# Optimization experiments

Measured on AMD Instinct MI355X. Metric: run time of the kernel, lower is better.

Reference implementation:

```python
import jax, jax.numpy as jnp
import numpy as np

B, T, C, H = 2, 2048, 2048, 16
DH = C // H  # 128
INNER = 4 * C  # 8192
EPS = 1e-5


def _ln(x, w, b):
    mu = jnp.mean(x, axis=-1, keepdims=True)
    var = jnp.mean((x - mu) ** 2, axis=-1, keepdims=True)
    return (x - mu) * jax.lax.rsqrt(var + EPS) * w + b


def _apply_rotary(x, cos, sin):
    # x: [B,H,T,DH]; cos/sin: [T,DH//2] broadcast over B,H
    x1 = x[..., ::2]
    x2 = x[..., 1::2]
    r = jnp.stack([x1 * cos - x2 * sin, x1 * sin + x2 * cos], axis=-1)
    return r.reshape(r.shape[:-2] + (-1,))


def setup_inputs() -> dict:
    key = jax.random.key(0)
    ks = jax.random.split(key, 8)
    std = 0.02
    x = jax.random.normal(ks[0], (B, T, C), dtype=jnp.float32)
    # RoPE tables
    inv_freq = 1.0 / (10000.0 ** (np.arange(0, DH, 2, dtype=np.float32) / DH))
    ang = np.arange(T, dtype=np.float32)[:, None] * inv_freq[None, :]  # [T, DH//2]
    cos = jnp.asarray(np.cos(ang))
    sin = jnp.asarray(np.sin(ang))
    return {
        "x": x,
        "cos": cos,
        "sin": sin,
        "ln1_w": jnp.ones((C,), jnp.float32),
        "ln1_b": jnp.zeros((C,), jnp.float32),
        "ln2_w": jnp.ones((C,), jnp.float32),
        "ln2_b": jnp.zeros((C,), jnp.float32),
        "W_qkv": jax.random.normal(ks[1], (C, 3 * C), jnp.float32) * std,
        "W_o": jax.random.normal(ks[2], (C, C), jnp.float32) * std,
        "W1": jax.random.normal(ks[3], (C, INNER), jnp.float32) * std,
        "W2": jax.random.normal(ks[4], (C, INNER), jnp.float32) * std,
        "W3": jax.random.normal(ks[5], (INNER, C), jnp.float32) * std,
    }


def reference(x, cos, sin, ln1_w, ln1_b, ln2_w, ln2_b, W_qkv, W_o, W1, W2, W3):
    # --- attention sub-block (pre-LN) ---
    a = _ln(x, ln1_w, ln1_b)
    qkv = a @ W_qkv  # [B,T,3C]
    q, k, v = jnp.split(qkv, 3, axis=-1)
    q = q.reshape(B, T, H, DH).transpose(0, 2, 1, 3)  # [B,H,T,DH]
    k = k.reshape(B, T, H, DH).transpose(0, 2, 1, 3)
    v = v.reshape(B, T, H, DH).transpose(0, 2, 1, 3)
    q = _apply_rotary(q, cos, sin)
    k = _apply_rotary(k, cos, sin)
    scores = jnp.einsum("bhtd,bhsd->bhts", q, k) / jnp.sqrt(jnp.float32(DH))
    mask = jnp.triu(jnp.full((T, T), -jnp.inf, dtype=scores.dtype), k=1)
    scores = scores + mask
    attn = jax.nn.softmax(scores, axis=-1)
    y = jnp.einsum("bhts,bhsd->bhtd", attn, v)
    y = y.transpose(0, 2, 1, 3).reshape(B, T, C) @ W_o
    x = x + y
    # --- SwiGLU MLP sub-block (pre-LN) ---
    h = _ln(x, ln2_w, ln2_b)
    m = (jax.nn.silu(h @ W1) * (h @ W2)) @ W3
    return x + m
```

## Files before the change

### kernel.cpp

```cpp
#include <hip/hip_runtime.h>
#include <hip/hip_bf16.h>
#include <cstdint>

#define DEVINL __device__ __forceinline__

using f32x4  = __attribute__((ext_vector_type(4))) float;
using short8 = __attribute__((ext_vector_type(8))) short;
using short4v = __attribute__((ext_vector_type(4))) short;

DEVINL float bf2f(__hip_bfloat16 h){ return __bfloat162float(h); }
DEVINL __hip_bfloat16 f2bf(float f){ return __float2bfloat16(f); }
DEVINL short bfbits(float f){ __hip_bfloat16 h = __float2bfloat16(f); short s; __builtin_memcpy(&s, &h, 2); return s; }
DEVINL float sb2f(short s){ uint32_t u = ((uint32_t)(uint16_t)s) << 16; float f; __builtin_memcpy(&f, &u, 4); return f; }

DEVINL void gl_lds16(const void* g, void* l){
  __builtin_amdgcn_global_load_lds((const __attribute__((address_space(1))) void*)g,
                                   (__attribute__((address_space(3))) void*)l, 16, 0, 0);
}

__global__ __launch_bounds__(256) void wtrans(const float* __restrict__ src,
                                              __hip_bfloat16* __restrict__ dst,
                                              int R, int C){
  __shared__ float tile[32][33];
  const int tr0 = blockIdx.y*32, tc0 = blockIdx.x*32;
  const int t = threadIdx.x;
  const int lr = t >> 3, lc = (t & 7) * 4;
  float4 v = *(const float4*)(src + (size_t)(tr0+lr)*C + tc0 + lc);
  tile[lr][lc] = v.x; tile[lr][lc+1] = v.y; tile[lr][lc+2] = v.z; tile[lr][lc+3] = v.w;
  __syncthreads();
  short4v o;
  o[0] = bfbits(tile[lc+0][lr]);
  o[1] = bfbits(tile[lc+1][lr]);
  o[2] = bfbits(tile[lc+2][lr]);
  o[3] = bfbits(tile[lc+3][lr]);
  *(short4v*)(dst + (size_t)(tc0+lr)*R + tr0 + lc) = o;
}

__global__ __launch_bounds__(256) void ln_k(const float* __restrict__ x,
                                            const float* __restrict__ w,
                                            const float* __restrict__ bia,
                                            __hip_bfloat16* __restrict__ out){
  const int row = blockIdx.x, t = threadIdx.x;
  const float* xr = x + (size_t)row*2048;
  float4 v0 = *(const float4*)(xr + t*4);
  float4 v1 = *(const float4*)(xr + 1024 + t*4);
  float s  = v0.x+v0.y+v0.z+v0.w + v1.x+v1.y+v1.z+v1.w;
  float ss = v0.x*v0.x+v0.y*v0.y+v0.z*v0.z+v0.w*v0.w
           + v1.x*v1.x+v1.y*v1.y+v1.z*v1.z+v1.w*v1.w;
  #pragma unroll
  for (int o=1;o<64;o<<=1){ s += __shfl_xor(s,o); ss += __shfl_xor(ss,o); }
  __shared__ float red[8];
  const int wv = t>>6, ln = t&63;
  if (ln==0){ red[wv]=s; red[4+wv]=ss; }
  __syncthreads();
  s = red[0]+red[1]+red[2]+red[3]; ss = red[4]+red[5]+red[6]+red[7];
  const float mu = s*(1.f/2048.f);
  const float inv = rsqrtf(ss*(1.f/2048.f) - mu*mu + 1e-5f);
  {
    float4 wv4 = *(const float4*)(w + t*4);
    float4 bv4 = *(const float4*)(bia + t*4);
    short4v o;
    o[0]=bfbits((v0.x-mu)*inv*wv4.x + bv4.x);
    o[1]=bfbits((v0.y-mu)*inv*wv4.y + bv4.y);
    o[2]=bfbits((v0.z-mu)*inv*wv4.z + bv4.z);
    o[3]=bfbits((v0.w-mu)*inv*wv4.w + bv4.w);
    *(short4v*)(out + (size_t)row*2048 + t*4) = o;
  }
  {
    float4 wv4 = *(const float4*)(w + 1024 + t*4);
    float4 bv4 = *(const float4*)(bia + 1024 + t*4);
    short4v o;
    o[0]=bfbits((v1.x-mu)*inv*wv4.x + bv4.x);
    o[1]=bfbits((v1.y-mu)*inv*wv4.y + bv4.y);
    o[2]=bfbits((v1.z-mu)*inv*wv4.z + bv4.z);
    o[3]=bfbits((v1.w-mu)*inv*wv4.w + bv4.w);
    *(short4v*)(out + (size_t)row*2048 + 1024 + t*4) = o;
  }
}

template<int EPI, int BM>
__global__ __launch_bounds__(512, 2) void gemmq(
    const __hip_bfloat16* __restrict__ A,
    const __hip_bfloat16* __restrict__ Bt,
    __hip_bfloat16* __restrict__ Cb,
    float* __restrict__ Cf,
    const float* __restrict__ resid,
    const __hip_bfloat16* __restrict__ emul,
    int M, int N, int K, int NTN)
{
  constexpr int MF    = BM/32;
  constexpr int LA    = BM/128;
  constexpr int ABY   = BM*64;
  constexpr int TILEB = ABY + 16384;
  extern __shared__ char smem[];
  const int tid = threadIdx.x, lane = tid & 63, wave = tid >> 6;
  const int l15 = lane & 15, l4 = lane >> 4;
  const int wm = wave >> 2, wn = wave & 3;

  const int id  = blockIdx.x;
  const int xcd = id & 7, jj = id >> 3, cpx = NTN >> 3;
  const int bx = xcd*cpx + jj % cpx, by = jj / cpx;
  const int row0 = by * BM, col0 = bx * 256;

  const __hip_bfloat16* srcA[LA]; int dstA[LA];
  #pragma unroll
  for (int g = 0; g < LA; ++g){
    const int c = g*512 + tid, r = c >> 2, s = c & 3;
    const int colb = (s << 4) ^ ((r & 3) << 4);
    srcA[g] = A + (size_t)(row0 + r)*K + (colb >> 1);
    dstA[g] = c*16;
  }
  const __hip_bfloat16* srcB[2]; int dstB[2];
  #pragma unroll
  for (int g = 0; g < 2; ++g){
    const int c = g*512 + tid, r = c >> 2, s = c & 3;
    const int colb = (s << 4) ^ ((r & 3) << 4);
    srcB[g] = Bt + (size_t)(col0 + r)*K + (colb >> 1);
    dstB[g] = c*16;
  }
  auto STAGE = [&](int bi, int kt){
    char* base = smem + bi*TILEB;
    #pragma unroll
    for (int g = 0; g < LA; ++g) gl_lds16(srcA[g] + kt*32, base + dstA[g]);
    #pragma unroll
    for (int g = 0; g < 2; ++g)  gl_lds16(srcB[g] + kt*32, base + ABY + dstB[g]);
  };

  int offA[MF], offB[4];
  #pragma unroll
  for (int m = 0; m < MF; ++m){
    const int r = wm*(BM/2) + m*16 + l15;
    offA[m] = r*64 + ((l4*16) ^ ((r & 3) << 4));
  }
  #pragma unroll
  for (int n = 0; n < 4; ++n){
    const int r = wn*64 + n*16 + l15;
    offB[n] = r*64 + ((l4*16) ^ ((r & 3) << 4));
  }

  f32x4 acc[MF][4] = {};
  const int NT = K >> 5;

  STAGE(0, 0); STAGE(1, 1); STAGE(2, 2);
  __builtin_amdgcn_sched_barrier(0);
  if constexpr (BM == 256) asm volatile("s_waitcnt vmcnt(8)" ::: "memory");
  else                     asm volatile("s_waitcnt vmcnt(6)" ::: "memory");
  __builtin_amdgcn_s_barrier();
  __builtin_amdgcn_sched_barrier(0);

  for (int t = 0; t < NT; ++t){
    const char* base = smem + (t & 3)*TILEB;
    short8 a[MF], b[4];
    #pragma unroll
    for (int m = 0; m < MF; ++m) a[m] = *(const short8*)(base + offA[m]);
    #pragma unroll
    for (int n = 0; n < 4; ++n)  b[n] = *(const short8*)(base + ABY + offB[n]);
    __builtin_amdgcn_s_setprio(1);
    #pragma unroll
    for (int m = 0; m < MF; ++m)
      #pragma unroll
      for (int n = 0; n < 4; ++n)
        acc[m][n] = __builtin_amdgcn_mfma_f32_16x16x32_bf16(a[m], b[n], acc[m][n], 0, 0, 0);
    __builtin_amdgcn_s_setprio(0);
    __builtin_amdgcn_sched_barrier(0);
    __builtin_amdgcn_s_barrier();
    __builtin_amdgcn_sched_barrier(0);
    if (t + 3 < NT){
      STAGE((t + 3) & 3, t + 3);
      __builtin_amdgcn_sched_barrier(0);
      if constexpr (BM == 256) asm volatile("s_waitcnt vmcnt(8)" ::: "memory");
      else                     asm volatile("s_waitcnt vmcnt(6)" ::: "memory");
    } else {
      asm volatile("s_waitcnt vmcnt(0)" ::: "memory");
    }
    __builtin_amdgcn_s_barrier();
    __builtin_amdgcn_sched_barrier(0);
  }

  #pragma unroll
  for (int m = 0; m < MF; ++m){
    const int r0 = row0 + wm*(BM/2) + m*16 + l4*4;
    #pragma unroll
    for (int n = 0; n < 4; ++n){
      const int c = col0 + wn*64 + n*16 + l15;
      #pragma unroll
      for (int j = 0; j < 4; ++j){
        const size_t idx = (size_t)(r0 + j)*N + c;
        const float v = acc[m][n][j];
        if constexpr (EPI == 1)      Cf[idx] = v + resid[idx];
        else if constexpr (EPI == 2) Cb[idx] = f2bf(v / (1.f + __expf(-v)));
        else if constexpr (EPI == 3) Cb[idx] = f2bf(v * bf2f(emul[idx]));
        else                         Cb[idx] = f2bf(v);
      }
    }
  }
}

__global__ __launch_bounds__(256) void ropepack(
    const __hip_bfloat16* __restrict__ qkv, const float* __restrict__ cosT, const float* __restrict__ sinT,
    __hip_bfloat16* __restrict__ Qo, __hip_bfloat16* __restrict__ Ko, __hip_bfloat16* __restrict__ Vo)
{
  __shared__ short vt[128][72];
  const int bh = blockIdx.y, b = bh>>4, h = bh&15;
  const int t0 = blockIdx.x*64, tid = threadIdx.x;
  const int tr = tid>>2, q4 = tid&3;
  const int tg = t0 + tr;
  const __hip_bfloat16* base = qkv + ((size_t)(b*2048 + tg))*6144 + h*128;
  const int pp0 = q4*16;
  float cs[16], sn[16];
  #pragma unroll
  for (int i=0;i<4;i++){
    float4 c4 = *(const float4*)(cosT + (size_t)tg*64 + pp0 + i*4);
    float4 s4 = *(const float4*)(sinT + (size_t)tg*64 + pp0 + i*4);
    cs[i*4+0]=c4.x; cs[i*4+1]=c4.y; cs[i*4+2]=c4.z; cs[i*4+3]=c4.w;
    sn[i*4+0]=s4.x; sn[i*4+1]=s4.y; sn[i*4+2]=s4.z; sn[i*4+3]=s4.w;
  }
  #pragma unroll
  for (int qk=0; qk<2; ++qk){
    const __hip_bfloat16* src = base + qk*2048;
    __hip_bfloat16* dst = (qk==0 ? Qo : Ko) + ((size_t)bh*2048 + tg)*128 + pp0*2;
    short8 ov[4];
    short* o = (short*)ov;
    #pragma unroll
    for (int i=0;i<4;i++){
      short8 v = *(const short8*)(src + pp0*2 + i*8);
      #pragma unroll
      for (int j=0;j<4;j++){
        float xe = sb2f(v[2*j]), xo = sb2f(v[2*j+1]);
        float c = cs[4*i+j], s = sn[4*i+j];
        o[8*i+2*j]   = bfbits(xe*c - xo*s);
        o[8*i+2*j+1] = bfbits(xe*s + xo*c);
      }
    }
    #pragma unroll
    for (int i=0;i<4;i++) *(short8*)(dst + i*8) = ov[i];
  }
  const __hip_bfloat16* vsrc = base + 4096;
  const int vc0 = q4*32;
  #pragma unroll
  for (int i=0;i<4;i++){
    short8 v = *(const short8*)(vsrc + vc0 + i*8);
    #pragma unroll
    for (int j=0;j<8;j++) vt[vc0+i*8+j][tr] = v[j];
  }
  __syncthreads();
  const int d = tid>>1, th0 = (tid&1)*32;
  __hip_bfloat16* vdst = Vo + ((size_t)bh*128 + d)*2048 + t0 + th0;
  #pragma unroll
  for (int i=0;i<4;i++)
    *(short8*)(vdst + i*8) = *(const short8*)(&vt[d][th0 + i*8]);
}

__global__ __launch_bounds__(512, 2) void attn_k(
    const __hip_bfloat16* __restrict__ Q,
    const __hip_bfloat16* __restrict__ K,
    const __hip_bfloat16* __restrict__ Vt,
    __hip_bfloat16* __restrict__ Y)
{
  extern __shared__ char lds[];
  const int bh = blockIdx.x, b = bh>>4, h = bh&15;
  const int by = blockIdx.y;
  const int qtA = 15 - 2*by, qtB = 2*by;
  const int tid = threadIdx.x, lane = tid&63, wave = tid>>6;
  const int qt = (wave < 4) ? qtA : qtB;
  const int qbase = qt*128 + (wave&3)*32;
  const int qmax = (qtA > qtB) ? qtA : qtB;
  const int nsteps = 2*qmax + 2;
  const __hip_bfloat16* Qh = Q + (size_t)bh*2048*128;
  const __hip_bfloat16* Kh = K + (size_t)bh*2048*128;
  const __hip_bfloat16* Vh = Vt + (size_t)bh*128*2048;
  char* plbase = lds + 65536 + wave*4608;
  const int l15 = lane & 15, l4 = lane >> 4;
  const int swzm = (l15 & 7) << 4;

  const int krA = tid >> 4;  const int kjA = (tid & 15) * 16;
  const size_t ksrcA = (size_t)krA*128 + ((kjA ^ ((krA & 7) << 4)) >> 1);
  const size_t ksrcB = (size_t)(krA+32)*128 + ((kjA ^ ((krA & 7) << 4)) >> 1);
  const int vrA = tid >> 3;  const int vjA = (tid & 7) * 16;
  const size_t vsrcA = (size_t)vrA*2048 + ((vjA ^ ((vrA & 7) << 4)) >> 1);
  const size_t vsrcB = (size_t)(vrA+64)*2048 + ((vjA ^ ((vrA & 7) << 4)) >> 1);
  auto STAGE = [&](int buf, int kv0){
    char* kb = lds + buf*16384;
    char* vb = lds + 32768 + buf*16384;
    gl_lds16(Kh + (size_t)kv0*128 + ksrcA, kb + tid*16);
    gl_lds16(Kh + (size_t)kv0*128 + ksrcB, kb + 8192 + tid*16);
    gl_lds16(Vh + kv0 + vsrcA, vb + tid*16);
    gl_lds16(Vh + kv0 + vsrcB, vb + 8192 + tid*16);
  };

  short8 qf[2][4];
  #pragma unroll
  for (int m=0;m<2;m++)
    #pragma unroll
    for (int kc=0;kc<4;kc++)
      qf[m][kc] = *(const short8*)(Qh + (size_t)(qbase + m*16 + l15)*128 + kc*32 + l4*8);

  short8 of;
  #pragma unroll
  for (int i=0;i<8;i++) of[i] = (l15==0) ? (short)0x3F80 : (short)0;

  f32x4 accO[2][9] = {};
  float mrow[2][4];
  #pragma unroll
  for (int m=0;m<2;m++)
    #pragma unroll
    for (int j=0;j<4;j++) mrow[m][j] = -1e30f;
  const float scale = 0.08838834764831845f;

  STAGE(0, 0);
  STAGE(1, 64);
  __builtin_amdgcn_sched_barrier(0);
  asm volatile("s_waitcnt vmcnt(4)" ::: "memory");
  __builtin_amdgcn_s_barrier();
  __builtin_amdgcn_sched_barrier(0);

  for (int s = 0; s < nsteps; ++s){
    const int kv0 = s*64;
    const char* kb = lds + (s&1)*16384;
    const char* vb = lds + 32768 + (s&1)*16384;
    if (kv0 <= qbase){
      const bool diag = (kv0 + 64 > qbase);
      const int kvrel = kv0 - qbase;
      f32x4 sc[2][4] = {};
      #pragma unroll
      for (int n=0;n<4;n++){
        short8 kf[4];
        #pragma unroll
        for (int kc=0;kc<4;kc++)
          kf[kc] = *(const short8*)(kb + (n*16 + l15)*256 + ((kc*64 + l4*16) ^ swzm));
        #pragma unroll
        for (int m=0;m<2;m++)
          #pragma unroll
          for (int kc=0;kc<4;kc++)
            sc[m][n] = __builtin_amdgcn_mfma_f32_16x16x32_bf16(qf[m][kc], kf[kc], sc[m][n], 0,0,0);
      }
      float alpha_[2][4];
      #pragma unroll
      for (int m=0;m<2;m++)
        #pragma unroll
        for (int j=0;j<4;j++){
          const int qr = 16*m + 4*l4 + j;
          float a[4];
          #pragma unroll
          for (int n=0;n<4;n++){
            a[n] = sc[m][n][j]*scale;
            if (diag && (kvrel + n*16 + l15 > qr)) a[n] = -1e30f;
          }
          float mx = fmaxf(fmaxf(a[0],a[1]), fmaxf(a[2],a[3]));
          #pragma unroll
          for (int o=1;o<16;o<<=1) mx = fmaxf(mx, __shfl_xor(mx, o));
          const float mn = fmaxf(mrow[m][j], mx);
          const float al = __expf(mrow[m][j] - mn);
          mrow[m][j] = mn;
          alpha_[m][j] = al;
          __hip_bfloat16* pr = (__hip_bfloat16*)(plbase + qr*144) + l15;
          #pragma unroll
          for (int n=0;n<4;n++) pr[n*16] = f2bf(__expf(a[n] - mn));
        }
      #pragma unroll
      for (int m=0;m<2;m++)
        #pragma unroll
        for (int db=0;db<9;db++)
          #pragma unroll
          for (int j=0;j<4;j++)
            accO[m][db][j] *= alpha_[m][j];
      asm volatile("s_waitcnt lgkmcnt(0)" ::: "memory");
      __builtin_amdgcn_sched_barrier(0);
      short8 pa[2][2];
      #pragma unroll
      for (int m=0;m<2;m++)
        #pragma unroll
        for (int ks=0;ks<2;ks++)
          pa[m][ks] = *(const short8*)(plbase + (m*16 + l15)*144 + ks*64 + l4*16);
      #pragma unroll
      for (int db=0;db<8;db++){
        #pragma unroll
        for (int ks=0;ks<2;ks++){
          short8 vf = *(const short8*)(vb + (db*16 + l15)*128 + ((ks*64 + l4*16) ^ swzm));
          #pragma unroll
          for (int m=0;m<2;m++)
            accO[m][db] = __builtin_amdgcn_mfma_f32_16x16x32_bf16(pa[m][ks], vf, accO[m][db], 0,0,0);
        }
      }
      #pragma unroll
      for (int ks=0;ks<2;ks++)
        #pragma unroll
        for (int m=0;m<2;m++)
          accO[m][8] = __builtin_amdgcn_mfma_f32_16x16x32_bf16(pa[m][ks], of, accO[m][8], 0,0,0);
    }
    __builtin_amdgcn_sched_barrier(0);
    __builtin_amdgcn_s_barrier();
    __builtin_amdgcn_sched_barrier(0);
    if (s + 2 < nsteps){
      STAGE(s&1, (s+2)*64);
      __builtin_amdgcn_sched_barrier(0);
      asm volatile("s_waitcnt vmcnt(4)" ::: "memory");
    } else {
      asm volatile("s_waitcnt vmcnt(0)" ::: "memory");
    }
    __builtin_amdgcn_s_barrier();
    __builtin_amdgcn_sched_barrier(0);
  }

  #pragma unroll
  for (int m=0;m<2;m++){
    float lr[4];
    #pragma unroll
    for (int j=0;j<4;j++) lr[j] = __shfl(accO[m][8][j], l4*16);
    #pragma unroll
    for (int db=0;db<8;db++)
      #pragma unroll
      for (int j=0;j<4;j++){
        const int tg = qbase + 16*m + 4*l4 + j;
        const int d  = 16*db + l15;
        Y[((size_t)b*2048 + tg)*2048 + h*128 + d] = f2bf(accO[m][db][j] / lr[j]);
      }
  }
}

extern "C" void kernel_launch(void* const* d_in, const int* in_sizes, int n_in,
                              void* d_out, int out_size, void* d_ws, size_t ws_size,
                              hipStream_t stream)
{
  const float* x    = (const float*)d_in[0];
  const float* cosT = (const float*)d_in[1];
  const float* sinT = (const float*)d_in[2];
  const float* ln1w = (const float*)d_in[3];
  const float* ln1b = (const float*)d_in[4];
  const float* ln2w = (const float*)d_in[5];
  const float* ln2b = (const float*)d_in[6];
  const float* Wqkv = (const float*)d_in[7];
  const float* Wo   = (const float*)d_in[8];
  const float* W1   = (const float*)d_in[9];
  const float* W2   = (const float*)d_in[10];
  const float* W3   = (const float*)d_in[11];
  float* out = (float*)d_out;

  if (ws_size < 150994944) return;
  char* ws = (char*)d_ws;
  __hip_bfloat16* WT   = (__hip_bfloat16*)(ws);
  __hip_bfloat16* abf  = (__hip_bfloat16*)(ws + 33554432);
  __hip_bfloat16* qkvb = (__hip_bfloat16*)(ws + 50331648);
  __hip_bfloat16* Yb   = (__hip_bfloat16*)(ws + 50331648);
  __hip_bfloat16* sub  = (__hip_bfloat16*)(ws + 50331648);
  __hip_bfloat16* Qb   = (__hip_bfloat16*)(ws + 100663296);
  __hip_bfloat16* Kb   = (__hip_bfloat16*)(ws + 117440512);
  __hip_bfloat16* Vtb  = (__hip_bfloat16*)(ws + 134217728);
  float*          x2   = out;

  hipFuncSetAttribute(reinterpret_cast<const void*>(&gemmq<4,256>),
                      hipFuncAttributeMaxDynamicSharedMemorySize, 131072);
  hipFuncSetAttribute(reinterpret_cast<const void*>(&gemmq<2,256>),
                      hipFuncAttributeMaxDynamicSharedMemorySize, 131072);
  hipFuncSetAttribute(reinterpret_cast<const void*>(&gemmq<3,256>),
                      hipFuncAttributeMaxDynamicSharedMemorySize, 131072);
  hipFuncSetAttribute(reinterpret_cast<const void*>(&gemmq<1,128>),
                      hipFuncAttributeMaxDynamicSharedMemorySize, 98304);
  hipFuncSetAttribute(reinterpret_cast<const void*>(&attn_k),
                      hipFuncAttributeMaxDynamicSharedMemorySize, 102400);

  ln_k<<<4096,256,0,stream>>>(x, ln1w, ln1b, abf);
  wtrans<<<dim3(192,64),256,0,stream>>>(Wqkv, WT, 2048, 6144);
  gemmq<4,256><<<384,512,131072,stream>>>(abf, WT, qkvb, nullptr, nullptr, nullptr, 4096, 6144, 2048, 24);
  ropepack<<<dim3(32,32),256,0,stream>>>(qkvb, cosT, sinT, Qb, Kb, Vtb);
  attn_k<<<dim3(32,8),512,102400,stream>>>(Qb, Kb, Vtb, Yb);
  wtrans<<<dim3(64,64),256,0,stream>>>(Wo, WT, 2048, 2048);
  gemmq<1,128><<<256,512,98304,stream>>>(Yb, WT, nullptr, x2, x, nullptr, 4096, 2048, 2048, 8);
  ln_k<<<4096,256,0,stream>>>(x2, ln2w, ln2b, abf);
  wtrans<<<dim3(256,64),256,0,stream>>>(W1, WT, 2048, 8192);
  gemmq<2,256><<<512,512,131072,stream>>>(abf, WT, sub, nullptr, nullptr, nullptr, 4096, 8192, 2048, 32);
  wtrans<<<dim3(256,64),256,0,stream>>>(W2, WT, 2048, 8192);
  gemmq<3,256><<<512,512,131072,stream>>>(abf, WT, sub, nullptr, nullptr, sub, 4096, 8192, 2048, 32);
  wtrans<<<dim3(64,256),256,0,stream>>>(W3, WT, 8192, 2048);
  gemmq<1,128><<<256,512,98304,stream>>>(sub, WT, nullptr, out, x2, nullptr, 4096, 2048, 8192, 8);
}
```

Measured before the change: 868.0 us.

## Restructure GEMM pipeline: early prefetch, single barrier, new swizzles, smaller QKV tiles

```diff
diff --git a/kernel.cpp b/kernel.cpp
--- a/kernel.cpp
+++ b/kernel.cpp
@@ -79,7 +79,7 @@
 }
 
 template<int EPI, int BM>
-__global__ __launch_bounds__(512, 2) void gemmq(
+__global__ __launch_bounds__(512, 2) void gemmp(
     const __hip_bfloat16* __restrict__ A,
     const __hip_bfloat16* __restrict__ Bt,
     __hip_bfloat16* __restrict__ Cb,
@@ -97,25 +97,26 @@
   const int l15 = lane & 15, l4 = lane >> 4;
   const int wm = wave >> 2, wn = wave & 3;
 
+  const int nwg = gridDim.x;
   const int id  = blockIdx.x;
-  const int xcd = id & 7, jj = id >> 3, cpx = NTN >> 3;
-  const int bx = xcd*cpx + jj % cpx, by = jj / cpx;
+  const int swz = (id & 7) * (nwg >> 3) + (id >> 3);
+  const int by = swz / NTN, bx = swz % NTN;
   const int row0 = by * BM, col0 = bx * 256;
 
   const __hip_bfloat16* srcA[LA]; int dstA[LA];
   #pragma unroll
   for (int g = 0; g < LA; ++g){
     const int c = g*512 + tid, r = c >> 2, s = c & 3;
-    const int colb = (s << 4) ^ ((r & 3) << 4);
-    srcA[g] = A + (size_t)(row0 + r)*K + (colb >> 1);
+    const int kbyte = (s*16) ^ (((r >> 1) & 3) << 4);
+    srcA[g] = A + (size_t)(row0 + r)*K + (kbyte >> 1);
     dstA[g] = c*16;
   }
   const __hip_bfloat16* srcB[2]; int dstB[2];
   #pragma unroll
   for (int g = 0; g < 2; ++g){
     const int c = g*512 + tid, r = c >> 2, s = c & 3;
-    const int colb = (s << 4) ^ ((r & 3) << 4);
-    srcB[g] = Bt + (size_t)(col0 + r)*K + (colb >> 1);
+    const int kbyte = (s*16) ^ (((r >> 1) & 3) << 4);
+    srcB[g] = Bt + (size_t)(col0 + r)*K + (kbyte >> 1);
     dstB[g] = c*16;
   }
   auto STAGE = [&](int bi, int kt){
@@ -126,16 +127,17 @@
     for (int g = 0; g < 2; ++g)  gl_lds16(srcB[g] + kt*32, base + ABY + dstB[g]);
   };
 
+  const int rmask = ((l15 >> 1) & 3) << 4;
   int offA[MF], offB[4];
   #pragma unroll
   for (int m = 0; m < MF; ++m){
     const int r = wm*(BM/2) + m*16 + l15;
-    offA[m] = r*64 + ((l4*16) ^ ((r & 3) << 4));
+    offA[m] = r*64 + ((l4*16) ^ rmask);
   }
   #pragma unroll
   for (int n = 0; n < 4; ++n){
     const int r = wn*64 + n*16 + l15;
-    offB[n] = r*64 + ((l4*16) ^ ((r & 3) << 4));
+    offB[n] = r*64 + ((l4*16) ^ rmask);
   }
 
   f32x4 acc[MF][4] = {};
@@ -150,6 +152,7 @@
 
   for (int t = 0; t < NT; ++t){
     const char* base = smem + (t & 3)*TILEB;
+    if (t + 3 < NT) STAGE((t + 3) & 3, t + 3);
     short8 a[MF], b[4];
     #pragma unroll
     for (int m = 0; m < MF; ++m) a[m] = *(const short8*)(base + offA[m]);
@@ -162,14 +165,12 @@
       for (int n = 0; n < 4; ++n)
         acc[m][n] = __builtin_amdgcn_mfma_f32_16x16x32_bf16(a[m], b[n], acc[m][n], 0, 0, 0);
     __builtin_amdgcn_s_setprio(0);
-    __builtin_amdgcn_sched_barrier(0);
-    __builtin_amdgcn_s_barrier();
-    __builtin_amdgcn_sched_barrier(0);
     if (t + 3 < NT){
-      STAGE((t + 3) & 3, t + 3);
-      __builtin_amdgcn_sched_barrier(0);
       if constexpr (BM == 256) asm volatile("s_waitcnt vmcnt(8)" ::: "memory");
       else                     asm volatile("s_waitcnt vmcnt(6)" ::: "memory");
+    } else if (t + 2 < NT){
+      if constexpr (BM == 256) asm volatile("s_waitcnt vmcnt(4)" ::: "memory");
+      else                     asm volatile("s_waitcnt vmcnt(3)" ::: "memory");
     } else {
       asm volatile("s_waitcnt vmcnt(0)" ::: "memory");
     }
@@ -448,29 +449,29 @@
   __hip_bfloat16* Vtb  = (__hip_bfloat16*)(ws + 134217728);
   float*          x2   = out;
 
-  hipFuncSetAttribute(reinterpret_cast<const void*>(&gemmq<4,256>),
+  hipFuncSetAttribute(reinterpret_cast<const void*>(&gemmp<4,128>),
+                      hipFuncAttributeMaxDynamicSharedMemorySize, 98304);
+  hipFuncSetAttribute(reinterpret_cast<const void*>(&gemmp<2,256>),
                       hipFuncAttributeMaxDynamicSharedMemorySize, 131072);
-  hipFuncSetAttribute(reinterpret_cast<const void*>(&gemmq<2,256>),
+  hipFuncSetAttribute(reinterpret_cast<const void*>(&gemmp<3,256>),
                       hipFuncAttributeMaxDynamicSharedMemorySize, 131072);
-  hipFuncSetAttribute(reinterpret_cast<const void*>(&gemmq<3,256>),
-                      hipFuncAttributeMaxDynamicSharedMemorySize, 131072);
-  hipFuncSetAttribute(reinterpret_cast<const void*>(&gemmq<1,128>),
+  hipFuncSetAttribute(reinterpret_cast<const void*>(&gemmp<1,128>),
                       hipFuncAttributeMaxDynamicSharedMemorySize, 98304);
   hipFuncSetAttribute(reinterpret_cast<const void*>(&attn_k),
                       hipFuncAttributeMaxDynamicSharedMemorySize, 102400);
 
   ln_k<<<4096,256,0,stream>>>(x, ln1w, ln1b, abf);
   wtrans<<<dim3(192,64),256,0,stream>>>(Wqkv, WT, 2048, 6144);
-  gemmq<4,256><<<384,512,131072,stream>>>(abf, WT, qkvb, nullptr, nullptr, nullptr, 4096, 6144, 2048, 24);
+  gemmp<4,128><<<768,512,98304,stream>>>(abf, WT, qkvb, nullptr, nullptr, nullptr, 4096, 6144, 2048, 24);
   ropepack<<<dim3(32,32),256,0,stream>>>(qkvb, cosT, sinT, Qb, Kb, Vtb);
   attn_k<<<dim3(32,8),512,102400,stream>>>(Qb, Kb, Vtb, Yb);
   wtrans<<<dim3(64,64),256,0,stream>>>(Wo, WT, 2048, 2048);
-  gemmq<1,128><<<256,512,98304,stream>>>(Yb, WT, nullptr, x2, x, nullptr, 4096, 2048, 2048, 8);
+  gemmp<1,128><<<256,512,98304,stream>>>(Yb, WT, nullptr, x2, x, nullptr, 4096, 2048, 2048, 8);
   ln_k<<<4096,256,0,stream>>>(x2, ln2w, ln2b, abf);
   wtrans<<<dim3(256,64),256,0,stream>>>(W1, WT, 2048, 8192);
-  gemmq<2,256><<<512,512,131072,stream>>>(abf, WT, sub, nullptr, nullptr, nullptr, 4096, 8192, 2048, 32);
+  gemmp<2,256><<<512,512,131072,stream>>>(abf, WT, sub, nullptr, nullptr, nullptr, 4096, 8192, 2048, 32);
   wtrans<<<dim3(256,64),256,0,stream>>>(W2, WT, 2048, 8192);
-  gemmq<3,256><<<512,512,131072,stream>>>(abf, WT, sub, nullptr, nullptr, sub, 4096, 8192, 2048, 32);
+  gemmp<3,256><<<512,512,131072,stream>>>(abf, WT, sub, nullptr, nullptr, sub, 4096, 8192, 2048, 32);
   wtrans<<<dim3(64,256),256,0,stream>>>(W3, WT, 8192, 2048);
-  gemmq<1,128><<<256,512,98304,stream>>>(sub, WT, nullptr, out, x2, nullptr, 4096, 2048, 8192, 8);
-}
+  gemmp<1,128><<<256,512,98304,stream>>>(sub, WT, nullptr, out, x2, nullptr, 4096, 2048, 8192, 8);
+}
```

Result: faster. 818.6 us (-5.7%).
